# Kernel tuning notes

Hardware: AMD Instinct MI355X
Metric: run time of the kernel (lower is better)

## Reference

```python
import jax, jax.numpy as jnp
import numpy as np


def setup_inputs() -> dict:
    key = jax.random.key(0)
    k1, k2, k3, k4, k5 = jax.random.split(key, 5)
    B, T, D, L = 8, 512, 512, 24
    V = 50000
    x = jax.random.normal(k1, (B, T, D), dtype=jnp.float32) * 0.1
    node_vecs = jax.random.normal(k2, (V - 1, D), dtype=jnp.float32) * 0.05
    paths = jax.random.randint(k3, (B, T, L), 0, V - 1, dtype=jnp.int32)
    codes = jax.random.randint(k4, (B, T, L), 0, 2, dtype=jnp.int32)
    mask = jax.random.randint(k5, (B, T, L), 0, 2, dtype=jnp.int32)
    return {"x": x, "node_vecs": node_vecs, "paths": paths, "codes": codes, "mask": mask}


def reference(x, node_vecs, paths, codes, mask):
    # x: [B, T, D] input word vectors
    # node_vecs: [V-1, D] Huffman internal-node parameters
    # paths: [B, T, L] internal-node indices along each target word's path
    # codes: [B, T, L] Huffman bits (0/1); mask: [B, T, L] valid-depth mask
    B = x.shape[0]
    path_vecs = node_vecs[paths]                     # [B, T, L, D] gather
    logits = jnp.einsum('btd,btld->btl', x, path_vecs)
    signs = 1.0 - 2.0 * codes.astype(x.dtype)        # bit 0 -> +1, bit 1 -> -1
    # per-node -log sigmoid(sign * logit); sum over path, words; avg over sequences
    node_nll = -jax.nn.log_sigmoid(signs * logits) * mask.astype(x.dtype)
    return jnp.sum(node_nll) / B
```

## Files before the change

kernel.cpp:

```cpp
#include <hip/hip_runtime.h>

#define BB 8
#define TT 512
#define DD 512
#define LL 24
#define WPB 8
#define LPW 3
#define NBLK (BB * TT)
#define NPART (NBLK * WPB)

typedef float vf4 __attribute__((ext_vector_type(4)));

__global__ __launch_bounds__(512, 8) void hs_kernel(
    const float* __restrict__ x,
    const float* __restrict__ node_vecs,
    const int* __restrict__ paths,
    const int* __restrict__ codes,
    const int* __restrict__ mask,
    float* __restrict__ partials)
{
    const int bt   = blockIdx.x;
    const int tid  = threadIdx.x;
    const int lane = tid & 63;
    const int wave = __builtin_amdgcn_readfirstlane(tid >> 6);

    const int base = bt * LL + wave * LPW;

    int msk[LPW], cod[LPW], pth[LPW];
    #pragma unroll
    for (int j = 0; j < LPW; ++j) {
        msk[j] = mask[base + j];
        cod[j] = codes[base + j];
        pth[j] = paths[base + j];
    }

    const vf4* xg = (const vf4*)(x + (size_t)bt * DD);
    const vf4 b0 = xg[lane];
    const vf4 b1 = xg[lane + 64];

    vf4 a0[LPW], a1[LPW];
    #pragma unroll
    for (int j = 0; j < LPW; ++j) {
        if (msk[j]) {
            const vf4* nv = (const vf4*)(node_vecs + (size_t)pth[j] * DD);
            a0[j] = __builtin_nontemporal_load(&nv[lane]);
            a1[j] = __builtin_nontemporal_load(&nv[lane + 64]);
        } else {
            a0[j] = (vf4)(0.0f);
            a1[j] = (vf4)(0.0f);
        }
    }

    float dot[LPW];
    #pragma unroll
    for (int j = 0; j < LPW; ++j) {
        dot[j] = a0[j].x * b0.x + a0[j].y * b0.y + a0[j].z * b0.z + a0[j].w * b0.w
               + a1[j].x * b1.x + a1[j].y * b1.y + a1[j].z * b1.z + a1[j].w * b1.w;
    }

    #pragma unroll
    for (int off = 32; off >= 1; off >>= 1) {
        #pragma unroll
        for (int j = 0; j < LPW; ++j)
            dot[j] += __shfl_xor(dot[j], off, 64);
    }

    float local = 0.0f;
    #pragma unroll
    for (int j = 0; j < LPW; ++j) {
        const float z   = (2.0f * (float)cod[j] - 1.0f) * dot[j];
        const float e   = __expf(-fabsf(z));
        const float nll = fmaxf(z, 0.0f) + __logf(1.0f + e);
        local += msk[j] ? nll : 0.0f;
    }

    if (lane == 0) __builtin_nontemporal_store(local, &partials[bt * WPB + wave]);
}

__global__ __launch_bounds__(1024) void hs_reduce(
    const float* __restrict__ partials, float* __restrict__ out)
{
    const int tid  = threadIdx.x;
    const int lane = tid & 63;
    const int wave = tid >> 6;
    __shared__ float wsum[16];

    const vf4* p4 = (const vf4*)partials;
    float s = 0.0f;
    #pragma unroll
    for (int r = 0; r < 8; ++r) {
        const vf4 v = p4[tid + r * 1024];
        s += (v.x + v.y) + (v.z + v.w);
    }

    #pragma unroll
    for (int off = 32; off >= 1; off >>= 1)
        s += __shfl_xor(s, off, 64);

    if (lane == 0) wsum[wave] = s;
    __syncthreads();
    if (tid == 0) {
        float t = 0.0f;
        #pragma unroll
        for (int i = 0; i < 16; ++i) t += wsum[i];
        out[0] = t * (1.0f / (float)BB);
    }
}

extern "C" void kernel_launch(void* const* d_in, const int* in_sizes, int n_in,
                              void* d_out, int out_size, void* d_ws, size_t ws_size,
                              hipStream_t stream) {
    const float* x         = (const float*)d_in[0];
    const float* node_vecs = (const float*)d_in[1];
    const int*   paths     = (const int*)d_in[2];
    const int*   codes     = (const int*)d_in[3];
    const int*   mask      = (const int*)d_in[4];
    float*       out       = (float*)d_out;
    float*       partials  = (float*)d_ws;

    hs_kernel<<<NBLK, 512, 0, stream>>>(x, node_vecs, paths, codes, mask, partials);
    hs_reduce<<<1, 1024, 0, stream>>>(partials, out);
}
```

Measured before the change: 159.0 us.

## Give each wave 12 path nodes with double-buffered gather prefetch

Changes the work split from eight waves with three nodes each per (b,t) to two waves with twelve nodes each, launched as 256-thread blocks. Each wave now loads x once per twelve nodes instead of once per three, and software-pipelines node-vector gathers so the next three rows load while the current three are reduced. The partial count shrinks to match and the reduce kernel reads fewer values. Nontemporal loads and stores are dropped. Fewer waves in flight means less latency hiding through occupancy, which the register double-buffering has to make up for.

```diff
diff --git a/kernel.cpp b/kernel.cpp
--- a/kernel.cpp
+++ b/kernel.cpp
@@ -4,14 +4,13 @@
 #define TT 512
 #define DD 512
 #define LL 24
-#define WPB 8
-#define LPW 3
-#define NBLK (BB * TT)
-#define NPART (NBLK * WPB)
+#define NBT (BB * TT)
+#define NWAVE (NBT * 2)
+#define NPART NWAVE
 
 typedef float vf4 __attribute__((ext_vector_type(4)));
 
-__global__ __launch_bounds__(512, 8) void hs_kernel(
+__global__ __launch_bounds__(256, 4) void hs_kernel(
     const float* __restrict__ x,
     const float* __restrict__ node_vecs,
     const int* __restrict__ paths,
@@ -19,62 +18,78 @@
     const int* __restrict__ mask,
     float* __restrict__ partials)
 {
-    const int bt   = blockIdx.x;
     const int tid  = threadIdx.x;
     const int lane = tid & 63;
     const int wave = __builtin_amdgcn_readfirstlane(tid >> 6);
+    const int wid  = blockIdx.x * 4 + wave;
+    const int bt   = wid >> 1;
+    const int lb   = bt * LL + (wid & 1) * 12;
 
-    const int base = bt * LL + wave * LPW;
-
-    int msk[LPW], cod[LPW], pth[LPW];
+    int msk[12], cod[12], pth[12];
     #pragma unroll
-    for (int j = 0; j < LPW; ++j) {
-        msk[j] = mask[base + j];
-        cod[j] = codes[base + j];
-        pth[j] = paths[base + j];
+    for (int l = 0; l < 12; ++l) {
+        msk[l] = mask[lb + l];
+        cod[l] = codes[lb + l];
+        pth[l] = paths[lb + l];
     }
 
     const vf4* xg = (const vf4*)(x + (size_t)bt * DD);
     const vf4 b0 = xg[lane];
     const vf4 b1 = xg[lane + 64];
 
-    vf4 a0[LPW], a1[LPW];
-    #pragma unroll
-    for (int j = 0; j < LPW; ++j) {
-        if (msk[j]) {
-            const vf4* nv = (const vf4*)(node_vecs + (size_t)pth[j] * DD);
-            a0[j] = __builtin_nontemporal_load(&nv[lane]);
-            a1[j] = __builtin_nontemporal_load(&nv[lane + 64]);
-        } else {
-            a0[j] = (vf4)(0.0f);
-            a1[j] = (vf4)(0.0f);
-        }
-    }
-
-    float dot[LPW];
-    #pragma unroll
-    for (int j = 0; j < LPW; ++j) {
-        dot[j] = a0[j].x * b0.x + a0[j].y * b0.y + a0[j].z * b0.z + a0[j].w * b0.w
-               + a1[j].x * b1.x + a1[j].y * b1.y + a1[j].z * b1.z + a1[j].w * b1.w;
-    }
+    vf4 gA[2][3], gB[2][3];
 
     #pragma unroll
-    for (int off = 32; off >= 1; off >>= 1) {
-        #pragma unroll
-        for (int j = 0; j < LPW; ++j)
-            dot[j] += __shfl_xor(dot[j], off, 64);
+    for (int k = 0; k < 3; ++k) {
+        if (msk[k]) {
+            const vf4* nv = (const vf4*)(node_vecs + (size_t)pth[k] * DD);
+            gA[0][k] = nv[lane];
+            gB[0][k] = nv[lane + 64];
+        } else { gA[0][k] = (vf4)(0.0f); gB[0][k] = (vf4)(0.0f); }
     }
 
     float local = 0.0f;
     #pragma unroll
-    for (int j = 0; j < LPW; ++j) {
-        const float z   = (2.0f * (float)cod[j] - 1.0f) * dot[j];
-        const float e   = __expf(-fabsf(z));
-        const float nll = fmaxf(z, 0.0f) + __logf(1.0f + e);
-        local += msk[j] ? nll : 0.0f;
+    for (int i = 0; i < 4; ++i) {
+        const int cb = i & 1, nb = cb ^ 1;
+
+        if (i < 3) {
+            #pragma unroll
+            for (int k = 0; k < 3; ++k) {
+                const int l = (i + 1) * 3 + k;
+                if (msk[l]) {
+                    const vf4* nv = (const vf4*)(node_vecs + (size_t)pth[l] * DD);
+                    gA[nb][k] = nv[lane];
+                    gB[nb][k] = nv[lane + 64];
+                } else { gA[nb][k] = (vf4)(0.0f); gB[nb][k] = (vf4)(0.0f); }
+            }
+        }
+
+        float dot[3];
+        #pragma unroll
+        for (int k = 0; k < 3; ++k) {
+            dot[k] = gA[cb][k].x * b0.x + gA[cb][k].y * b0.y
+                   + gA[cb][k].z * b0.z + gA[cb][k].w * b0.w
+                   + gB[cb][k].x * b1.x + gB[cb][k].y * b1.y
+                   + gB[cb][k].z * b1.z + gB[cb][k].w * b1.w;
+        }
+        #pragma unroll
+        for (int off = 32; off >= 1; off >>= 1) {
+            #pragma unroll
+            for (int k = 0; k < 3; ++k)
+                dot[k] += __shfl_xor(dot[k], off, 64);
+        }
+        #pragma unroll
+        for (int k = 0; k < 3; ++k) {
+            const int l = i * 3 + k;
+            const float z   = (2.0f * (float)cod[l] - 1.0f) * dot[k];
+            const float e   = __expf(-fabsf(z));
+            const float nll = fmaxf(z, 0.0f) + __logf(1.0f + e);
+            local += msk[l] ? nll : 0.0f;
+        }
     }
 
-    if (lane == 0) __builtin_nontemporal_store(local, &partials[bt * WPB + wave]);
+    if (lane == 0) partials[wid] = local;
 }
 
 __global__ __launch_bounds__(1024) void hs_reduce(
@@ -88,7 +103,7 @@
     const vf4* p4 = (const vf4*)partials;
     float s = 0.0f;
     #pragma unroll
-    for (int r = 0; r < 8; ++r) {
+    for (int r = 0; r < 2; ++r) {
         const vf4 v = p4[tid + r * 1024];
         s += (v.x + v.y) + (v.z + v.w);
     }
@@ -118,6 +133,6 @@
     float*       out       = (float*)d_out;
     float*       partials  = (float*)d_ws;
 
-    hs_kernel<<<NBLK, 512, 0, stream>>>(x, node_vecs, paths, codes, mask, partials);
+    hs_kernel<<<NWAVE / 4, 256, 0, stream>>>(x, node_vecs, paths, codes, mask, partials);
     hs_reduce<<<1, 1024, 0, stream>>>(partials, out);
 }
```

Result: no change. 159.5 us (+0.3%).
